# Optimization experiments

Hardware: AMD Instinct MI355X
Metric: run time of the kernel (lower is better)

## Reference

```python
import jax, jax.numpy as jnp
import numpy as np

B, D_IN, D_HID, D_OUT, E = 8192, 1024, 4096, 1024, 8


def setup_inputs() -> dict:
    key = jax.random.key(0)
    ks = jax.random.split(key, 6)
    s_in = 1.0 / np.sqrt(D_IN)
    s_gh = 1.0 / np.sqrt(D_HID // 2)
    s_eh = 1.0 / np.sqrt(D_HID)
    return {
        "x": jax.random.normal(ks[0], (B, D_IN), jnp.float32),
        "gW1": jax.random.normal(ks[1], (D_IN, D_HID // 2), jnp.float32) * s_in,
        "gb1": jnp.zeros((D_HID // 2,), jnp.float32),
        "gW2": jax.random.normal(ks[2], (D_HID // 2, E), jnp.float32) * s_gh,
        "gb2": jnp.zeros((E,), jnp.float32),
        "eW1": jax.random.normal(ks[3], (E, D_IN, D_HID), jnp.float32) * s_in,
        "eb1": jnp.zeros((E, D_HID), jnp.float32),
        "eW2": jax.random.normal(ks[4], (E, D_HID, D_OUT), jnp.float32) * s_eh,
        "eb2": jnp.zeros((E, D_OUT), jnp.float32),
    }


def reference(x, gW1, gb1, gW2, gb2, eW1, eb1, eW2, eb2):
    # Gating network: Linear -> ReLU -> (Dropout: eval identity) -> Linear -> Softmax(dim=1)
    gh = jax.nn.relu(x @ gW1 + gb1)                      # [B, H/2]
    gates = jax.nn.softmax(gh @ gW2 + gb2, axis=1)       # [B, E]

    # All experts run on the full batch (dense MoE): batched GEMMs over expert axis.
    h = jax.nn.relu(jnp.einsum('bi,eih->beh', x, eW1) + eb1)   # [B, E, H]
    eo = jnp.einsum('beh,eho->beo', h, eW2) + eb2              # [B, E, O]

    # Gated weighted sum over experts.
    combined = jnp.einsum('beo,be->bo', eo, gates)             # [B, O]
    return (combined, gates, gates)
```

## Files before the change

### kernel.cpp

```cpp
#include <hip/hip_runtime.h>
#include <hip/hip_bf16.h>
#include <stdint.h>

#define BB 8192
#define DIN 1024
#define DHID 4096
#define DOUT 1024
#define NEXP 8
#define GH_N 2048

typedef __attribute__((ext_vector_type(8))) __bf16 bf16x8;
typedef __attribute__((ext_vector_type(4))) float f32x4;

__device__ inline unsigned short f2bf(float f) {
  unsigned u = __builtin_bit_cast(unsigned, f);
  u = (u + 0x7FFFu + ((u >> 16) & 1u)) >> 16;
  return (unsigned short)u;
}
__device__ inline float b2f(unsigned short s) {
  return __builtin_bit_cast(float, (unsigned)s << 16);
}

__global__ void cvt_f32_bf16(const float* __restrict__ in,
                             unsigned short* __restrict__ out, int n4) {
  int i = blockIdx.x * blockDim.x + threadIdx.x;
  if (i >= n4) return;
  float4 v = ((const float4*)in)[i];
  ushort4 o;
  o.x = f2bf(v.x); o.y = f2bf(v.y); o.z = f2bf(v.z); o.w = f2bf(v.w);
  ((ushort4*)out)[i] = o;
}

__device__ inline void tr128(const float* __restrict__ in,
                             unsigned short* __restrict__ out, int R, int C,
                             int bx, int by, int t) {
  __shared__ float tile[128][65];
  const int c0 = bx * 64, r0 = by * 128;
  const int tx = t & 63, ty = t >> 6;
#pragma unroll
  for (int i = 0; i < 16; ++i) {
    int r = i * 8 + ty;
    tile[r][tx] = in[(size_t)(r0 + r) * C + c0 + tx];
  }
  __syncthreads();
  const int tx2 = t & 127, ty2 = t >> 7;
#pragma unroll
  for (int i = 0; i < 16; ++i) {
    int cc = i * 4 + ty2;
    out[(size_t)(c0 + cc) * R + r0 + tx2] = f2bf(tile[tx2][cc]);
  }
}

__global__ __launch_bounds__(512)
void trans_g(const float* __restrict__ gW1, unsigned short* __restrict__ gW1T) {
  int b = blockIdx.x;
  tr128(gW1, gW1T, DIN, GH_N, b & 31, b >> 5, threadIdx.x);
}

__global__ __launch_bounds__(512)
void trans2(const float* __restrict__ w1, unsigned short* __restrict__ w1T,
            const float* __restrict__ w2, unsigned short* __restrict__ w2T) {
  int b = blockIdx.x;
  if (b < 512) {
    tr128(w1, w1T, DIN, DHID, b & 63, b >> 6, threadIdx.x);
  } else {
    b -= 512;
    tr128(w2, w2T, DHID, DOUT, b & 15, b >> 4, threadIdx.x);
  }
}

__device__ inline void gload16(const void* g, void* l) {
  __builtin_amdgcn_global_load_lds(
      (const __attribute__((address_space(1))) void*)g,
      (__attribute__((address_space(3))) void*)l, 16, 0, 0);
}

template <int N>
__device__ inline void waitv() {
  if constexpr (N == 0) asm volatile("s_waitcnt vmcnt(0)" ::: "memory");
  else if constexpr (N == 2) asm volatile("s_waitcnt vmcnt(2)" ::: "memory");
  else if constexpr (N == 4) asm volatile("s_waitcnt vmcnt(4)" ::: "memory");
  else if constexpr (N == 6) asm volatile("s_waitcnt vmcnt(6)" ::: "memory");
  else asm volatile("s_waitcnt vmcnt(0)" ::: "memory");
}
__device__ inline void waitlgkm0() {
  asm volatile("s_waitcnt lgkmcnt(0)" ::: "memory");
  __builtin_amdgcn_sched_barrier(0);
}
__device__ inline bf16x8 ldr(const char* p) { return *(const bf16x8*)p; }

struct GArgs {
  const unsigned short* A;
  const unsigned short* Bt;
  int lda, ldb, N, K;
  const float* bias;
  unsigned short* outb;
  int nb;
};

__global__ __launch_bounds__(512, 2)
void gemmU(GArgs g) {
  __shared__ char lds[131072];
  char* Als = lds;
  char* Bls = lds + 65536;
  constexpr int ABYTES = 32768, BBYTES = 32768;
  const int t = threadIdx.x;
  const int lane = t & 63;
  const int wid = t >> 6;
  const int wm = wid >> 2;
  const int wn = wid & 3;
  const int l15 = lane & 15, lg = lane >> 4;

  const int nb = g.nb;
  const int local = blockIdx.x;
  const int swz = (local & 7) * (nb >> 3) + (local >> 3);
  const int nbn = g.N >> 8;
  const int bn = swz % nbn, bm = swz / nbn;
  const int m0 = bm * 256, n0 = bn * 256;

  const int prow = t >> 3;
  const int cOff = ((t & 7) ^ (prow & 7)) * 8;
  const unsigned short* aP[4];
  const unsigned short* bP[4];
#pragma unroll
  for (int u = 0; u < 4; ++u) {
    int p = u * 64 + prow;
    int ga = ((p >> 6) & 1) * 128 + ((p >> 7) & 1) * 64 + (p & 63);
    aP[u] = g.A + (size_t)(m0 + ga) * g.lda + cOff;
    int gb = ((p >> 5) & 3) * 64 + ((p >> 7) & 1) * 32 + (p & 31);
    bP[u] = g.Bt + (size_t)(n0 + gb) * g.ldb + cOff;
  }
  const int ldst = t * 16;

  const int slot0 = ((lg) ^ (l15 & 7)) * 16;
  const int slot1 = ((4 + lg) ^ (l15 & 7)) * 16;
  const int aRB0 = (wm * 64 + l15) * 128;
  const int aRB1 = (128 + wm * 64 + l15) * 128;
  const int bCB0 = (wn * 32 + l15) * 128;
  const int bCB1 = (128 + wn * 32 + l15) * 128;

  f32x4 acc[8][4];
  const f32x4 zero = {0.f, 0.f, 0.f, 0.f};
#pragma unroll
  for (int i = 0; i < 8; ++i)
#pragma unroll
    for (int j = 0; j < 4; ++j) acc[i][j] = zero;

  bf16x8 ar[4][2], bc0[2][2], bc1[2][2];
  const int NT = g.K >> 6;

  gload16(bP[0], Bls + 0 * 8192 + ldst);
  gload16(bP[1], Bls + 1 * 8192 + ldst);
  gload16(aP[0], Als + 0 * 8192 + ldst);
  gload16(aP[1], Als + 1 * 8192 + ldst);
  gload16(bP[2], Bls + 2 * 8192 + ldst);
  gload16(bP[3], Bls + 3 * 8192 + ldst);
  gload16(aP[2], Als + 2 * 8192 + ldst);
  gload16(aP[3], Als + 3 * 8192 + ldst);
  waitv<4>();
  __builtin_amdgcn_s_barrier();

  for (int T = 0; T < NT; ++T) {
    const int buf = T & 1;
    const char* Ab = Als + buf * ABYTES;
    const char* Bb = Bls + buf * BBYTES;
    char* An = Als + (buf ^ 1) * ABYTES;
    char* Bn = Bls + (buf ^ 1) * BBYTES;
    const bool stg = (T + 1 < NT);
    const int kn = (T + 1) << 6;

#pragma unroll
    for (int f = 0; f < 4; ++f) {
      ar[f][0] = ldr(Ab + aRB0 + f * 2048 + slot0);
      ar[f][1] = ldr(Ab + aRB0 + f * 2048 + slot1);
    }
#pragma unroll
    for (int c = 0; c < 2; ++c) {
      bc0[c][0] = ldr(Bb + bCB0 + c * 2048 + slot0);
      bc0[c][1] = ldr(Bb + bCB0 + c * 2048 + slot1);
    }
    if (stg) {
      gload16(bP[0] + kn, Bn + 0 * 8192 + ldst);
      gload16(bP[1] + kn, Bn + 1 * 8192 + ldst);
    }
    __builtin_amdgcn_s_barrier();
    waitlgkm0();
    __builtin_amdgcn_s_setprio(1);
#pragma unroll
    for (int ksl = 0; ksl < 2; ++ksl)
#pragma unroll
      for (int f = 0; f < 4; ++f)
#pragma unroll
        for (int c = 0; c < 2; ++c)
          acc[f][c] = __builtin_amdgcn_mfma_f32_16x16x32_bf16(
              ar[f][ksl], bc0[c][ksl], acc[f][c], 0, 0, 0);
    __builtin_amdgcn_s_setprio(0);
    if (stg) waitv<4>(); else waitv<2>();
    __builtin_amdgcn_s_barrier();

#pragma unroll
    for (int c = 0; c < 2; ++c) {
      bc1[c][0] = ldr(Bb + bCB1 + c * 2048 + slot0);
      bc1[c][1] = ldr(Bb + bCB1 + c * 2048 + slot1);
    }
    if (stg) {
      gload16(aP[0] + kn, An + 0 * 8192 + ldst);
      gload16(aP[1] + kn, An + 1 * 8192 + ldst);
    }
    __builtin_amdgcn_s_barrier();
    waitlgkm0();
    __builtin_amdgcn_s_setprio(1);
#pragma unroll
    for (int ksl = 0; ksl < 2; ++ksl)
#pragma unroll
      for (int f = 0; f < 4; ++f)
#pragma unroll
        for (int c = 0; c < 2; ++c)
          acc[f][2 + c] = __builtin_amdgcn_mfma_f32_16x16x32_bf16(
              ar[f][ksl], bc1[c][ksl], acc[f][2 + c], 0, 0, 0);
    __builtin_amdgcn_s_setprio(0);
    if (stg) waitv<4>(); else waitv<0>();
    __builtin_amdgcn_s_barrier();

#pragma unroll
    for (int f = 0; f < 4; ++f) {
      ar[f][0] = ldr(Ab + aRB1 + f * 2048 + slot0);
      ar[f][1] = ldr(Ab + aRB1 + f * 2048 + slot1);
    }
    if (stg) {
      gload16(bP[2] + kn, Bn + 2 * 8192 + ldst);
      gload16(bP[3] + kn, Bn + 3 * 8192 + ldst);
    }
    __builtin_amdgcn_s_barrier();
    waitlgkm0();
    __builtin_amdgcn_s_setprio(1);
#pragma unroll
    for (int ksl = 0; ksl < 2; ++ksl)
#pragma unroll
      for (int f = 0; f < 4; ++f)
#pragma unroll
        for (int c = 0; c < 2; ++c)
          acc[4 + f][2 + c] = __builtin_amdgcn_mfma_f32_16x16x32_bf16(
              ar[f][ksl], bc1[c][ksl], acc[4 + f][2 + c], 0, 0, 0);
    __builtin_amdgcn_s_setprio(0);
    __builtin_amdgcn_s_barrier();

    if (stg) {
      gload16(aP[2] + kn, An + 2 * 8192 + ldst);
      gload16(aP[3] + kn, An + 3 * 8192 + ldst);
    }
    __builtin_amdgcn_s_barrier();
    __builtin_amdgcn_s_setprio(1);
#pragma unroll
    for (int ksl = 0; ksl < 2; ++ksl)
#pragma unroll
      for (int f = 0; f < 4; ++f)
#pragma unroll
        for (int c = 0; c < 2; ++c)
          acc[4 + f][c] = __builtin_amdgcn_mfma_f32_16x16x32_bf16(
              ar[f][ksl], bc0[c][ksl], acc[4 + f][c], 0, 0, 0);
    __builtin_amdgcn_s_setprio(0);
    if (stg) waitv<4>();
    __builtin_amdgcn_s_barrier();
  }

  const int rb = m0 + wm * 128 + (lg << 2);
  const int cb = n0 + wn * 64 + l15;
  const int N = g.N;
#pragma unroll
  for (int fg = 0; fg < 8; ++fg) {
#pragma unroll
    for (int j = 0; j < 4; ++j) {
      int col = cb + j * 16;
      float bv = g.bias[col];
#pragma unroll
      for (int r = 0; r < 4; ++r) {
        int row = rb + fg * 16 + r;
        float v = acc[fg][j][r] + bv;
        g.outb[(size_t)row * N + col] = f2bf(fmaxf(v, 0.f));
      }
    }
  }
}

__global__ __launch_bounds__(512)
void gemmF(const unsigned short* __restrict__ A,
           const unsigned short* __restrict__ Bt,
           const float* __restrict__ bias,
           float* __restrict__ outC,
           const float* __restrict__ gates, int eidx, int accum) {
  constexpr int SLOT = 49152;
  __shared__ char lds[3 * SLOT];
  const int t = threadIdx.x;
  const int lane = t & 63;
  const int wid = t >> 6;
  const int wm = wid >> 2;
  const int wn = wid & 3;
  const int l15 = lane & 15, lg = lane >> 4;

  const int local = blockIdx.x;
  const int swz = (local & 7) * 32 + (local >> 3);
  const int bn = swz & 3, bm = swz >> 2;
  const int m0 = bm * 128, n0 = bn * 256;

  const int prow = t >> 3;
  const int cOff = ((t & 7) ^ (prow & 7)) * 8;
  const unsigned short* aP[2];
  const unsigned short* bP[4];
#pragma unroll
  for (int u = 0; u < 2; ++u)
    aP[u] = A + (size_t)(m0 + u * 64 + prow) * DHID + cOff;
#pragma unroll
  for (int u = 0; u < 4; ++u) {
    int p = u * 64 + prow;
    int gb = ((p >> 5) & 3) * 64 + ((p >> 7) & 1) * 32 + (p & 31);
    bP[u] = Bt + (size_t)(n0 + gb) * DHID + cOff;
  }
  const int ldst = t * 16;

  const int slot0 = ((lg) ^ (l15 & 7)) * 16;
  const int slot1 = ((4 + lg) ^ (l15 & 7)) * 16;
  const int aRB = (wm * 64 + l15) * 128;
  const int bCB0 = 16384 + (wn * 32 + l15) * 128;
  const int bCB1 = 16384 + (128 + wn * 32 + l15) * 128;

  f32x4 acc[4][4];
  const f32x4 zero = {0.f, 0.f, 0.f, 0.f};
#pragma unroll
  for (int i = 0; i < 4; ++i)
#pragma unroll
    for (int j = 0; j < 4; ++j) acc[i][j] = zero;

  bf16x8 af[2][2], bc[4][2];
  const int NT = DHID >> 6;

#pragma unroll
  for (int T0 = 0; T0 < 2; ++T0) {
    char* S = lds + T0 * SLOT;
    const int k0 = T0 << 6;
    gload16(aP[0] + k0, S + 0 * 8192 + ldst);
    gload16(aP[1] + k0, S + 1 * 8192 + ldst);
    gload16(bP[0] + k0, S + 16384 + 0 * 8192 + ldst);
    gload16(bP[1] + k0, S + 16384 + 1 * 8192 + ldst);
    gload16(bP[2] + k0, S + 16384 + 2 * 8192 + ldst);
    gload16(bP[3] + k0, S + 16384 + 3 * 8192 + ldst);
  }
  waitv<6>();
  __builtin_amdgcn_s_barrier();

  for (int T = 0; T < NT; ++T) {
    const char* Sb = lds + (T % 3) * SLOT;
    char* Sn = lds + ((T + 2) % 3) * SLOT;
    const bool stg = (T + 2 < NT);
    const int kn = (T + 2) << 6;

#pragma unroll
    for (int f = 0; f < 2; ++f) {
      af[f][0] = ldr(Sb + aRB + f * 2048 + slot0);
      af[f][1] = ldr(Sb + aRB + f * 2048 + slot1);
    }
#pragma unroll
    for (int c = 0; c < 2; ++c) {
      bc[c][0] = ldr(Sb + bCB0 + c * 2048 + slot0);
      bc[c][1] = ldr(Sb + bCB0 + c * 2048 + slot1);
      bc[2 + c][0] = ldr(Sb + bCB1 + c * 2048 + slot0);
      bc[2 + c][1] = ldr(Sb + bCB1 + c * 2048 + slot1);
    }
    if (stg) {
      gload16(aP[0] + kn, Sn + 0 * 8192 + ldst);
      gload16(aP[1] + kn, Sn + 1 * 8192 + ldst);
      gload16(bP[0] + kn, Sn + 16384 + 0 * 8192 + ldst);
    }
    __builtin_amdgcn_s_barrier();
    waitlgkm0();
    __builtin_amdgcn_s_setprio(1);
#pragma unroll
    for (int ksl = 0; ksl < 2; ++ksl)
#pragma unroll
      for (int f = 0; f < 2; ++f)
#pragma unroll
        for (int c = 0; c < 4; ++c)
          acc[f][c] = __builtin_amdgcn_mfma_f32_16x16x32_bf16(
              af[f][ksl], bc[c][ksl], acc[f][c], 0, 0, 0);
    __builtin_amdgcn_s_setprio(0);
    __builtin_amdgcn_s_barrier();

#pragma unroll
    for (int f = 0; f < 2; ++f) {
      af[f][0] = ldr(Sb + aRB + (2 + f) * 2048 + slot0);
      af[f][1] = ldr(Sb + aRB + (2 + f) * 2048 + slot1);
    }
    if (stg) {
      gload16(bP[1] + kn, Sn + 16384 + 1 * 8192 + ldst);
      gload16(bP[2] + kn, Sn + 16384 + 2 * 8192 + ldst);
      gload16(bP[3] + kn, Sn + 16384 + 3 * 8192 + ldst);
    }
    __builtin_amdgcn_s_barrier();
    waitlgkm0();
    __builtin_amdgcn_s_setprio(1);
#pragma unroll
    for (int ksl = 0; ksl < 2; ++ksl)
#pragma unroll
      for (int f = 0; f < 2; ++f)
#pragma unroll
        for (int c = 0; c < 4; ++c)
          acc[2 + f][c] = __builtin_amdgcn_mfma_f32_16x16x32_bf16(
              af[f][ksl], bc[c][ksl], acc[2 + f][c], 0, 0, 0);
    __builtin_amdgcn_s_setprio(0);
    if (stg) waitv<6>();
    else if (T + 1 < NT) waitv<0>();
    __builtin_amdgcn_s_barrier();
  }

  const int rb = m0 + wm * 64 + (lg << 2);
  const int cb = n0 + wn * 64 + l15;
#pragma unroll
  for (int fg = 0; fg < 4; ++fg) {
    float gv[4];
#pragma unroll
    for (int r = 0; r < 4; ++r)
      gv[r] = gates[(size_t)(rb + fg * 16 + r) * NEXP + eidx];
#pragma unroll
    for (int j = 0; j < 4; ++j) {
      int col = cb + j * 16;
      float bv = bias[col];
#pragma unroll
      for (int r = 0; r < 4; ++r) {
        size_t o = (size_t)(rb + fg * 16 + r) * DOUT + col;
        float v = (acc[fg][j][r] + bv) * gv[r];
        outC[o] = accum ? outC[o] + v : v;
      }
    }
  }
}

__global__ __launch_bounds__(512)
void gating_head2(const unsigned short* __restrict__ gh,
                  const float* __restrict__ gW2,
                  const float* __restrict__ gb2,
                  float* __restrict__ gws,
                  float* __restrict__ g1,
                  float* __restrict__ g2) {
  __shared__ float wT[8][2048];
  const int t = threadIdx.x;
  for (int idx = t; idx < 16384; idx += 512) {
    wT[idx & 7][idx >> 3] = gW2[idx];
  }
  __syncthreads();
  const int wid = t >> 6, lane = t & 63;
  const int row = blockIdx.x * 8 + wid;
  const unsigned short* ghr = gh + (size_t)row * 2048;
  float s[8] = {0.f, 0.f, 0.f, 0.f, 0.f, 0.f, 0.f, 0.f};
#pragma unroll
  for (int j = 0; j < 8; ++j) {
    int k4 = lane + 64 * j;
    ushort4 hv = ((const ushort4*)ghr)[k4];
    float h0 = b2f(hv.x), h1 = b2f(hv.y), h2 = b2f(hv.z), h3 = b2f(hv.w);
#pragma unroll
    for (int e = 0; e < 8; ++e) {
      float4 w = ((const float4*)&wT[e][0])[k4];
      s[e] += h0 * w.x + h1 * w.y + h2 * w.z + h3 * w.w;
    }
  }
#pragma unroll
  for (int e = 0; e < 8; ++e)
#pragma unroll
    for (int off = 1; off < 64; off <<= 1) s[e] += __shfl_xor(s[e], off, 64);
  if (lane == 0) {
    float l[8], m = -1e30f;
#pragma unroll
    for (int e = 0; e < 8; ++e) {
      l[e] = s[e] + gb2[e];
      m = fmaxf(m, l[e]);
    }
    float sum = 0.f;
#pragma unroll
    for (int e = 0; e < 8; ++e) {
      l[e] = expf(l[e] - m);
      sum += l[e];
    }
    float inv = 1.f / sum;
#pragma unroll
    for (int e = 0; e < 8; ++e) {
      float gv = l[e] * inv;
      gws[(size_t)row * 8 + e] = gv;
      g1[(size_t)row * 8 + e] = gv;
      g2[(size_t)row * 8 + e] = gv;
    }
  }
}

extern "C" void kernel_launch(void* const* d_in, const int* in_sizes, int n_in,
                              void* d_out, int out_size, void* d_ws,
                              size_t ws_size, hipStream_t stream) {
  (void)in_sizes; (void)n_in; (void)out_size; (void)ws_size;
  const float* x   = (const float*)d_in[0];
  const float* gW1 = (const float*)d_in[1];
  const float* gb1 = (const float*)d_in[2];
  const float* gW2 = (const float*)d_in[3];
  const float* gb2 = (const float*)d_in[4];
  const float* eW1 = (const float*)d_in[5];
  const float* eb1 = (const float*)d_in[6];
  const float* eW2 = (const float*)d_in[7];
  const float* eb2 = (const float*)d_in[8];

  float* outC  = (float*)d_out;
  float* outG1 = outC + (size_t)BB * DOUT;
  float* outG2 = outG1 + (size_t)BB * NEXP;

  char* ws = (char*)d_ws;
  unsigned short* xb   = (unsigned short*)(ws);
  float*          gat  = (float*)(ws + 16777216);
  unsigned short* w1T  = (unsigned short*)(ws + 17039360);
  unsigned short* w2T  = (unsigned short*)(ws + 25427968);
  unsigned short* hbuf = (unsigned short*)(ws + 33816576);
  unsigned short* gh   = hbuf;
  unsigned short* gW1T = w1T;

  cvt_f32_bf16<<<(BB * DIN / 4) / 256, 256, 0, stream>>>(x, xb, BB * DIN / 4);
  trans_g<<<256, 512, 0, stream>>>(gW1, gW1T);
  {
    GArgs a{xb, gW1T, DIN, DIN, GH_N, DIN, gb1, gh, 256};
    gemmU<<<256, 512, 0, stream>>>(a);
  }
  gating_head2<<<BB / 8, 512, 0, stream>>>(gh, gW2, gb2, gat, outG1, outG2);

  for (int e = 0; e < NEXP; ++e) {
    trans2<<<1024, 512, 0, stream>>>(
        eW1 + (size_t)e * DIN * DHID, w1T, eW2 + (size_t)e * DHID * DOUT, w2T);
    {
      GArgs a{xb, w1T, DIN, DIN, DHID, DIN, eb1 + (size_t)e * DHID, hbuf, 512};
      gemmU<<<512, 512, 0, stream>>>(a);
    }
    gemmF<<<256, 512, 0, stream>>>(hbuf, w2T, eb2 + (size_t)e * DOUT, outC,
                                   gat, e, e > 0 ? 1 : 0);
  }
}
```

Measured before the change: 1.346 ms.

## Load A fragments directly from global in second expert GEMM, shrink LDS pipeline

Result: slower. 2.142 ms (+59.1%).

```diff
diff --git a/kernel.cpp b/kernel.cpp
--- a/kernel.cpp
+++ b/kernel.cpp
@@ -80,7 +80,6 @@
   if constexpr (N == 0) asm volatile("s_waitcnt vmcnt(0)" ::: "memory");
   else if constexpr (N == 2) asm volatile("s_waitcnt vmcnt(2)" ::: "memory");
   else if constexpr (N == 4) asm volatile("s_waitcnt vmcnt(4)" ::: "memory");
-  else if constexpr (N == 6) asm volatile("s_waitcnt vmcnt(6)" ::: "memory");
   else asm volatile("s_waitcnt vmcnt(0)" ::: "memory");
 }
 __device__ inline void waitlgkm0() {
@@ -283,14 +282,14 @@
   }
 }
 
-__global__ __launch_bounds__(512)
-void gemmF(const unsigned short* __restrict__ A,
+__global__ __launch_bounds__(512, 4)
+void gemmR(const unsigned short* __restrict__ A,
            const unsigned short* __restrict__ Bt,
            const float* __restrict__ bias,
            float* __restrict__ outC,
            const float* __restrict__ gates, int eidx, int accum) {
-  constexpr int SLOT = 49152;
-  __shared__ char lds[3 * SLOT];
+  constexpr int SLOT = 32768;
+  __shared__ char lds[2 * SLOT];
   const int t = threadIdx.x;
   const int lane = t & 63;
   const int wid = t >> 6;
@@ -305,11 +304,7 @@
 
   const int prow = t >> 3;
   const int cOff = ((t & 7) ^ (prow & 7)) * 8;
-  const unsigned short* aP[2];
   const unsigned short* bP[4];
-#pragma unroll
-  for (int u = 0; u < 2; ++u)
-    aP[u] = A + (size_t)(m0 + u * 64 + prow) * DHID + cOff;
 #pragma unroll
   for (int u = 0; u < 4; ++u) {
     int p = u * 64 + prow;
@@ -320,9 +315,13 @@
 
   const int slot0 = ((lg) ^ (l15 & 7)) * 16;
   const int slot1 = ((4 + lg) ^ (l15 & 7)) * 16;
-  const int aRB = (wm * 64 + l15) * 128;
-  const int bCB0 = 16384 + (wn * 32 + l15) * 128;
-  const int bCB1 = 16384 + (128 + wn * 32 + l15) * 128;
+  const int bCB0 = (wn * 32 + l15) * 128;
+  const int bCB1 = (128 + wn * 32 + l15) * 128;
+
+  const unsigned short* aRow[4];
+#pragma unroll
+  for (int f = 0; f < 4; ++f)
+    aRow[f] = A + (size_t)(m0 + wm * 64 + f * 16 + l15) * DHID + lg * 8;
 
   f32x4 acc[4][4];
   const f32x4 zero = {0.f, 0.f, 0.f, 0.f};
@@ -334,31 +333,21 @@
   bf16x8 af[2][2], bc[4][2];
   const int NT = DHID >> 6;
 
-#pragma unroll
-  for (int T0 = 0; T0 < 2; ++T0) {
-    char* S = lds + T0 * SLOT;
-    const int k0 = T0 << 6;
-    gload16(aP[0] + k0, S + 0 * 8192 + ldst);
-    gload16(aP[1] + k0, S + 1 * 8192 + ldst);
-    gload16(bP[0] + k0, S + 16384 + 0 * 8192 + ldst);
-    gload16(bP[1] + k0, S + 16384 + 1 * 8192 + ldst);
-    gload16(bP[2] + k0, S + 16384 + 2 * 8192 + ldst);
-    gload16(bP[3] + k0, S + 16384 + 3 * 8192 + ldst);
-  }
-  waitv<6>();
+  {
+    char* S = lds;
+#pragma unroll
+    for (int u = 0; u < 4; ++u) gload16(bP[u], S + u * 8192 + ldst);
+  }
+  waitv<0>();
   __builtin_amdgcn_s_barrier();
 
   for (int T = 0; T < NT; ++T) {
-    const char* Sb = lds + (T % 3) * SLOT;
-    char* Sn = lds + ((T + 2) % 3) * SLOT;
-    const bool stg = (T + 2 < NT);
-    const int kn = (T + 2) << 6;
-
-#pragma unroll
-    for (int f = 0; f < 2; ++f) {
-      af[f][0] = ldr(Sb + aRB + f * 2048 + slot0);
-      af[f][1] = ldr(Sb + aRB + f * 2048 + slot1);
-    }
+    const char* Sb = lds + (T & 1) * SLOT;
+    char* Sn = lds + ((T + 1) & 1) * SLOT;
+    const bool stg = (T + 1 < NT);
+    const int kb = T << 6;
+    const int kn = (T + 1) << 6;
+
 #pragma unroll
     for (int c = 0; c < 2; ++c) {
       bc[c][0] = ldr(Sb + bCB0 + c * 2048 + slot0);
@@ -367,12 +356,15 @@
       bc[2 + c][1] = ldr(Sb + bCB1 + c * 2048 + slot1);
     }
     if (stg) {
-      gload16(aP[0] + kn, Sn + 0 * 8192 + ldst);
-      gload16(aP[1] + kn, Sn + 1 * 8192 + ldst);
-      gload16(bP[0] + kn, Sn + 16384 + 0 * 8192 + ldst);
-    }
-    __builtin_amdgcn_s_barrier();
-    waitlgkm0();
+#pragma unroll
+      for (int u = 0; u < 4; ++u) gload16(bP[u] + kn, Sn + u * 8192 + ldst);
+    }
+
+#pragma unroll
+    for (int f = 0; f < 2; ++f) {
+      af[f][0] = *(const bf16x8*)(aRow[f] + kb);
+      af[f][1] = *(const bf16x8*)(aRow[f] + kb + 32);
+    }
     __builtin_amdgcn_s_setprio(1);
 #pragma unroll
     for (int ksl = 0; ksl < 2; ++ksl)
@@ -383,20 +375,12 @@
           acc[f][c] = __builtin_amdgcn_mfma_f32_16x16x32_bf16(
               af[f][ksl], bc[c][ksl], acc[f][c], 0, 0, 0);
     __builtin_amdgcn_s_setprio(0);
-    __builtin_amdgcn_s_barrier();
 
 #pragma unroll
     for (int f = 0; f < 2; ++f) {
-      af[f][0] = ldr(Sb + aRB + (2 + f) * 2048 + slot0);
-      af[f][1] = ldr(Sb + aRB + (2 + f) * 2048 + slot1);
-    }
-    if (stg) {
-      gload16(bP[1] + kn, Sn + 16384 + 1 * 8192 + ldst);
-      gload16(bP[2] + kn, Sn + 16384 + 2 * 8192 + ldst);
-      gload16(bP[3] + kn, Sn + 16384 + 3 * 8192 + ldst);
-    }
-    __builtin_amdgcn_s_barrier();
-    waitlgkm0();
+      af[f][0] = *(const bf16x8*)(aRow[2 + f] + kb);
+      af[f][1] = *(const bf16x8*)(aRow[2 + f] + kb + 32);
+    }
     __builtin_amdgcn_s_setprio(1);
 #pragma unroll
     for (int ksl = 0; ksl < 2; ++ksl)
@@ -407,8 +391,8 @@
           acc[2 + f][c] = __builtin_amdgcn_mfma_f32_16x16x32_bf16(
               af[f][ksl], bc[c][ksl], acc[2 + f][c], 0, 0, 0);
     __builtin_amdgcn_s_setprio(0);
-    if (stg) waitv<6>();
-    else if (T + 1 < NT) waitv<0>();
+
+    if (stg) waitv<0>();
     __builtin_amdgcn_s_barrier();
   }
 
@@ -532,7 +516,7 @@
       GArgs a{xb, w1T, DIN, DIN, DHID, DIN, eb1 + (size_t)e * DHID, hbuf, 512};
       gemmU<<<512, 512, 0, stream>>>(a);
     }
-    gemmF<<<256, 512, 0, stream>>>(hbuf, w2T, eb2 + (size_t)e * DOUT, outC,
+    gemmR<<<256, 512, 0, stream>>>(hbuf, w2T, eb2 + (size_t)e * DOUT, outC,
                                    gat, e, e > 0 ? 1 : 0);
   }
 }
```
